# Kernel tuning notes

Hardware: AMD Instinct MI355X
Metric: run time of the kernel (lower is better)

## Reference

```python
import jax, jax.numpy as jnp
import numpy as np

DT = 0.1       # integration step (ms)
TAU_M = 10.0   # membrane time constant
TAU_S = 5.0    # synaptic time constant
E_REV = 1.0    # synaptic reversal potential
G_MAX = 1.0    # synaptic conductance scale
P, N, E, B, T = 8, 2048, 16, 4, 128


def setup_inputs() -> dict:
    key = jax.random.key(0)
    k_src, k_tgt, k_w, k_win = jax.random.split(key, 4)
    t_seq = jnp.arange(B * T, dtype=jnp.float32).reshape(B, T) * DT  # [B,T] times in ms
    src = jax.random.randint(k_src, (E,), 0, P, dtype=jnp.int32)
    tgt = jax.random.randint(k_tgt, (E,), 0, P, dtype=jnp.int32)
    W = jax.random.normal(k_w, (E, N, N), jnp.float32) * (1.0 / np.sqrt(N))
    W_in = jax.random.normal(k_win, (N, N), jnp.float32) * (1.0 / np.sqrt(N))
    v0 = jnp.zeros((P, B, N), jnp.float32)      # population states
    s0 = jnp.zeros((E, B, N), jnp.float32)      # recurrent synapse states
    s_in0 = jnp.zeros((B, N), jnp.float32)      # input synapse state
    return dict(t_seq=t_seq, W=W, W_in=W_in, v0=v0, s0=s0, s_in0=s_in0, src=src, tgt=tgt)


def _input_rate(t, n):
    # InputPopulation: firing rate is a pure function of time t, per-unit phase.
    phase = jnp.arange(n, dtype=jnp.float32) * (2.0 * jnp.pi / n)
    return 0.5 * (1.0 + jnp.sin(2.0 * jnp.pi * t[:, None] / 100.0 + phase[None, :]))  # [B,n]


def _simulate(t_seq, W, W_in, v0, s0, s_in0, src, tgt):
    n_pop = v0.shape[0]

    def step(carry, t):  # t: [B] current time
        v, s, s_in, err = carry
        rates = jax.nn.sigmoid(v)                      # [P,B,N] firing rates
        # --- synapse message passing: gather pre rates, dense projection ---
        pre = rates[src]                               # [E,B,N]
        drive = jnp.einsum('ebi,eij->ebj', pre, W)     # [E,B,N]
        s_new = s + DT * (-s / TAU_S + drive)          # exponential synapse state
        # --- input population synapse (pre rate is a function of t) ---
        rate_in = _input_rate(t, v.shape[-1])          # [B,N]
        s_in_new = s_in + DT * (-s_in / TAU_S + rate_in @ W_in)
        # --- conductance-based currents scattered into target populations ---
        post_v = v[tgt]                                # [E,B,N]
        I_e = G_MAX * s_new * (E_REV - post_v)
        g_e = G_MAX * s_new
        I_sum = jax.ops.segment_sum(I_e, tgt, num_segments=n_pop)  # [P,B,N]
        g_sum = jax.ops.segment_sum(g_e, tgt, num_segments=n_pop)
        I_in = G_MAX * s_in_new * (E_REV - v[0])
        I_sum = I_sum.at[0].add(I_in)
        g_sum = g_sum.at[0].add(G_MAX * s_in_new)
        # --- Euler integrator step + stability error accumulation ---
        dv = (-v - g_sum * v + I_sum) / TAU_M
        v_new = v + DT * dv
        err_new = err + jnp.mean(jnp.abs(dv)) * DT
        return (v_new, s_new, s_in_new, err_new), jax.nn.sigmoid(v_new)

    init = (v0, s0, s_in0, jnp.zeros((), jnp.float32))
    (v_f, s_f, s_in_f, err), rates_seq = jax.lax.scan(step, init, t_seq.T)  # rates_seq: [T,P,B,N]
    firing_rates = jnp.transpose(rates_seq, (2, 0, 1, 3))  # [B,T,P,N]
    return firing_rates, err


def reference(t_seq, W, W_in, v0, s0, s_in0, src, tgt):
    return _simulate(t_seq, W, W_in, v0, s0, s_in0, src, tgt)
```

## Files before the change

### kernel.cpp

```cpp
#include <hip/hip_runtime.h>
#include <math.h>

#define DT_     0.1f
#define TAU_M_  10.0f
#define TAU_S_  5.0f
#define NP_     8
#define NN_     2048
#define NE_     16
#define NB_     4
#define NT_     128
#define NEDGE_  17

typedef unsigned int u32;
typedef __attribute__((ext_vector_type(2))) _Float16 half2v;

__device__ __forceinline__ float sigmoidf_(float x) {
  return 1.0f / (1.0f + expf(-x));
}

__device__ __forceinline__ float dot2_(float acc, u32 p, u32 w) {
#if __has_builtin(__builtin_amdgcn_fdot2)
  return __builtin_amdgcn_fdot2(__builtin_bit_cast(half2v, p),
                                __builtin_bit_cast(half2v, w), acc, false);
#else
  half2v hp = __builtin_bit_cast(half2v, p);
  half2v hw = __builtin_bit_cast(half2v, w);
  return acc + (float)hp[0] * (float)hw[0] + (float)hp[1] * (float)hw[1];
#endif
}

__global__ __launch_bounds__(256) void k_transpose(
    const float* __restrict__ W, const float* __restrict__ W_in,
    u32* __restrict__ Wt32) {
  const int e  = blockIdx.x;
  const int jt = blockIdx.y;
  const int it = blockIdx.z;
  const float* Wsrc = (e == 16) ? W_in : (W + (size_t)e * NN_ * NN_);
  __shared__ float tile[64][65];
  const int i0 = it * 64, j0 = jt * 64;
  for (int k = threadIdx.x; k < 4096; k += 256) {
    int r = k >> 6, c = k & 63;
    tile[r][c] = Wsrc[(size_t)(i0 + r) * NN_ + j0 + c];
  }
  __syncthreads();
  for (int k = threadIdx.x; k < 2048; k += 256) {
    int jr = k >> 5, ip = k & 31;
    half2v h;
    h[0] = (_Float16)tile[2 * ip][jr];
    h[1] = (_Float16)tile[2 * ip + 1][jr];
    Wt32[((size_t)e * NN_ + (j0 + jr)) * 1024 + (i0 >> 1) + ip] =
        __builtin_bit_cast(u32, h);
  }
}

__global__ __launch_bounds__(256) void k_inrate(
    const float* __restrict__ t_seq, u32* __restrict__ inp) {
  const int t = blockIdx.x >> 2, b = blockIdx.x & 3;
  const float tt = t_seq[b * NT_ + t];
  const float base = 0.062831853071795864f * tt;
  for (int p2 = threadIdx.x; p2 < 1024; p2 += 256) {
    int i = 2 * p2;
    float ph0 = (float)i * (6.2831853071795864f / (float)NN_);
    float ph1 = (float)(i + 1) * (6.2831853071795864f / (float)NN_);
    half2v h;
    h[0] = (_Float16)(0.5f * (1.0f + sinf(base + ph0)));
    h[1] = (_Float16)(0.5f * (1.0f + sinf(base + ph1)));
    inp[(size_t)(t * NB_ + b) * 1024 + p2] = __builtin_bit_cast(u32, h);
  }
}

__global__ __launch_bounds__(256) void k_rates0(
    const float* __restrict__ v0, _Float16* __restrict__ rh0) {
  int idx = blockIdx.x * 256 + threadIdx.x;
  rh0[idx] = (_Float16)sigmoidf_(v0[idx]);
}

__global__ __launch_bounds__(256) void k_init(
    const float* __restrict__ v0, const float* __restrict__ s0,
    const float* __restrict__ s_in0,
    float* __restrict__ vg, float* __restrict__ sg,
    float* __restrict__ sig, float* __restrict__ errw) {
  int idx = blockIdx.x * 256 + threadIdx.x;
  if (idx < NE_ * NB_ * NN_) sg[idx] = s0[idx];
  if (idx < NP_ * NB_ * NN_) vg[idx] = v0[idx];
  if (idx < NB_ * NN_) sig[idx] = s_in0[idx];
  if (idx < NN_) errw[idx] = 0.0f;
}

__global__ __launch_bounds__(256) void k_step(
    const u32* __restrict__ Wt32, const u32* __restrict__ inp,
    const int* __restrict__ srcg, const int* __restrict__ tgtg,
    const u32* __restrict__ rcur, u32* __restrict__ rnext,
    float* __restrict__ sg_, float* __restrict__ sig_,
    float* __restrict__ vg_, float* __restrict__ errw,
    float* __restrict__ out, int t) {
  const int tid  = threadIdx.x;
  const int lane = tid & 63;
  const int wv   = tid >> 6;
  const int j    = blockIdx.x * 4 + wv;

  __shared__ u32 pairs_u[NB_ * 1024];

  float s_reg  = sg_[(size_t)lane * NN_ + j];
  float si_reg = (lane < 4) ? sig_[(size_t)lane * NN_ + j] : 0.0f;

  u32 streg[16];
  {
    const u32* rp = rcur + (size_t)srcg[0] * 4096 + tid * 16;
#pragma unroll
    for (int c = 0; c < 4; ++c) {
      uint4 q = *(const uint4*)(rp + c * 4);
      streg[c * 4 + 0] = q.x; streg[c * 4 + 1] = q.y;
      streg[c * 4 + 2] = q.z; streg[c * 4 + 3] = q.w;
    }
  }

  for (int E = 0; E < NEDGE_; ++E) {
    bool do_stage = (E == 0) || (E == 16) || (srcg[E] != srcg[E - 1]);
    if (do_stage) {
      __syncthreads();
#pragma unroll
      for (int c = 0; c < 4; ++c) {
        uint4 q = {streg[c * 4 + 0], streg[c * 4 + 1],
                   streg[c * 4 + 2], streg[c * 4 + 3]};
        *(uint4*)(&pairs_u[tid * 16 + c * 4]) = q;
      }
      __syncthreads();
    }
    if (E < 16) {
      bool next_stage = (E + 1 == 16) || (srcg[E + 1] != srcg[E]);
      if (next_stage) {
        const u32* np = (E + 1 == 16)
            ? (inp + (size_t)t * NB_ * 1024 + tid * 16)
            : (rcur + (size_t)srcg[E + 1] * 4096 + tid * 16);
#pragma unroll
        for (int c = 0; c < 4; ++c) {
          uint4 q = *(const uint4*)(np + c * 4);
          streg[c * 4 + 0] = q.x; streg[c * 4 + 1] = q.y;
          streg[c * 4 + 2] = q.z; streg[c * 4 + 3] = q.w;
        }
      }
    }

    const u32* wp = Wt32 + ((size_t)E * NN_ + j) * 1024;
    float acc0 = 0.0f, acc1 = 0.0f, acc2 = 0.0f, acc3 = 0.0f;
#pragma unroll
    for (int c = 0; c < 4; ++c) {
      const int base = c * 256 + lane * 4;
      uint4 w = *(const uint4*)(wp + base);
      uint4 p0 = *(const uint4*)(&pairs_u[base]);
      uint4 p1 = *(const uint4*)(&pairs_u[1024 + base]);
      uint4 p2 = *(const uint4*)(&pairs_u[2048 + base]);
      uint4 p3 = *(const uint4*)(&pairs_u[3072 + base]);
      acc0 = dot2_(dot2_(dot2_(dot2_(acc0, p0.x, w.x), p0.y, w.y), p0.z, w.z), p0.w, w.w);
      acc1 = dot2_(dot2_(dot2_(dot2_(acc1, p1.x, w.x), p1.y, w.y), p1.z, w.z), p1.w, w.w);
      acc2 = dot2_(dot2_(dot2_(dot2_(acc2, p2.x, w.x), p2.y, w.y), p2.z, w.z), p2.w, w.w);
      acc3 = dot2_(dot2_(dot2_(dot2_(acc3, p3.x, w.x), p3.y, w.y), p3.z, w.z), p3.w, w.w);
    }

    float t0 = acc0 + __shfl_xor(acc0, 1, 64);
    float t1 = acc1 + __shfl_xor(acc1, 1, 64);
    float t2 = acc2 + __shfl_xor(acc2, 1, 64);
    float t3 = acc3 + __shfl_xor(acc3, 1, 64);
    float u0 = (lane & 1) ? t1 : t0;
    float u2 = (lane & 1) ? t3 : t2;
    u0 = u0 + __shfl_xor(u0, 2, 64);
    u2 = u2 + __shfl_xor(u2, 2, 64);
    float r = (lane & 2) ? u2 : u0;
    r += __shfl_xor(r, 4, 64);
    r += __shfl_xor(r, 8, 64);
    r += __shfl_xor(r, 16, 64);
    r += __shfl_xor(r, 32, 64);

    if (E < NE_) {
      if ((lane >> 2) == E) s_reg += DT_ * (r - s_reg * (1.0f / TAU_S_));
    } else {
      if (lane < 4) si_reg += DT_ * (r - si_reg * (1.0f / TAU_S_));
    }
  }

  sg_[(size_t)lane * NN_ + j] = s_reg;
  if (lane < 4) sig_[(size_t)lane * NN_ + j] = si_reg;

  {
    const int p = lane >> 2, b = lane & 3;
    float S = 0.0f;
#pragma unroll
    for (int e = 0; e < NE_; ++e) {
      float se = __shfl(s_reg, e * 4 + b, 64);
      if (tgtg[e] == p) S += se;
    }
    float sival = __shfl(si_reg, b, 64);
    if (p == 0) S += sival;

    float vv = (lane < 32) ? vg_[(size_t)lane * NN_ + j] : 0.0f;
    float I  = S * (1.0f - vv);
    float dv = (-vv - S * vv + I) * (1.0f / TAU_M_);
    float vn = vv + DT_ * dv;
    float rr = sigmoidf_(vn);
    if (lane < 32) {
      vg_[(size_t)lane * NN_ + j] = vn;
      ((_Float16*)rnext)[(size_t)lane * NN_ + j] = (_Float16)rr;
      out[(((size_t)b * NT_ + t) * NP_ + p) * NN_ + j] = rr;
    }
    float ea = (lane < 32) ? fabsf(dv) : 0.0f;
#pragma unroll
    for (int off = 1; off < 64; off <<= 1) ea += __shfl_xor(ea, off, 64);
    if (lane == 0) errw[j] += ea;
  }
}

__global__ __launch_bounds__(256) void k_err(
    const float* __restrict__ errw, float* __restrict__ out_err) {
  __shared__ float red[256];
  float s = 0.0f;
  for (int k = threadIdx.x; k < NN_; k += 256) s += errw[k];
  red[threadIdx.x] = s;
  __syncthreads();
  for (int w = 128; w > 0; w >>= 1) {
    if (threadIdx.x < w) red[threadIdx.x] += red[threadIdx.x + w];
    __syncthreads();
  }
  if (threadIdx.x == 0)
    *out_err = red[0] * (DT_ / (float)(NP_ * NB_ * NN_));
}

extern "C" void kernel_launch(void* const* d_in, const int* in_sizes, int n_in,
                              void* d_out, int out_size, void* d_ws, size_t ws_size,
                              hipStream_t stream) {
  const float* t_seq = (const float*)d_in[0];
  const float* W     = (const float*)d_in[1];
  const float* W_in  = (const float*)d_in[2];
  const float* v0    = (const float*)d_in[3];
  const float* s0    = (const float*)d_in[4];
  const float* s_in0 = (const float*)d_in[5];
  const int*   srcp  = (const int*)d_in[6];
  const int*   tgtp  = (const int*)d_in[7];
  float* outp = (float*)d_out;

  u32* Wt32 = (u32*)d_ws;
  u32* inp  = Wt32 + (size_t)NEDGE_ * NN_ * 1024;
  u32* rb0  = inp + (size_t)NT_ * NB_ * 1024;
  u32* rb1  = rb0 + (size_t)NP_ * NB_ * 1024;
  float* sg   = (float*)(rb1 + (size_t)NP_ * NB_ * 1024);
  float* vg   = sg + (size_t)NE_ * NB_ * NN_;
  float* sig  = vg + (size_t)NP_ * NB_ * NN_;
  float* errw = sig + (size_t)NB_ * NN_;

  hipLaunchKernelGGL(k_transpose, dim3(NEDGE_, 32, 32), dim3(256), 0, stream,
                     W, W_in, Wt32);
  hipLaunchKernelGGL(k_inrate, dim3(NT_ * NB_), dim3(256), 0, stream,
                     t_seq, inp);
  hipLaunchKernelGGL(k_rates0, dim3(256), dim3(256), 0, stream,
                     v0, (_Float16*)rb0);
  hipLaunchKernelGGL(k_init, dim3(512), dim3(256), 0, stream,
                     v0, s0, s_in0, vg, sg, sig, errw);

  u32* rb[2] = {rb0, rb1};
  for (int t = 0; t < NT_; ++t) {
    hipLaunchKernelGGL(k_step, dim3(512), dim3(256), 0, stream,
                       Wt32, inp, srcp, tgtp,
                       rb[t & 1], rb[(t + 1) & 1],
                       sg, sig, vg, errw, outp, t);
  }

  hipLaunchKernelGGL(k_err, dim3(1), dim3(256), 0, stream,
                     errw, outp + (size_t)NB_ * NT_ * NP_ * NN_);
}
```

Before: 3.677 ms.

## Hold pre-rates in registers per wave and software-pipeline weight loads

Shared-memory staging of the pre-synaptic rates and its block barriers are removed. Each wave now loads the whole 4x1024 packed rate vector it needs straight into registers, with redundant global/L2 reads across the block's four waves. Weight rows for the next edge are prefetched into registers while the current edge's dot products run, and launch bounds request two blocks per CU. This raises register pressure (about 64 rate registers plus double-buffered weights), which could cause spills or lower occupancy.

```diff
diff --git a/kernel.cpp b/kernel.cpp
--- a/kernel.cpp
+++ b/kernel.cpp
@@ -87,7 +87,7 @@
   if (idx < NN_) errw[idx] = 0.0f;
 }
 
-__global__ __launch_bounds__(256) void k_step(
+__global__ __launch_bounds__(256, 2) void k_step(
     const u32* __restrict__ Wt32, const u32* __restrict__ inp,
     const int* __restrict__ srcg, const int* __restrict__ tgtg,
     const u32* __restrict__ rcur, u32* __restrict__ rnext,
@@ -98,64 +98,59 @@
   const int lane = tid & 63;
   const int wv   = tid >> 6;
   const int j    = blockIdx.x * 4 + wv;
-
-  __shared__ u32 pairs_u[NB_ * 1024];
+  const int l4   = lane * 4;
 
   float s_reg  = sg_[(size_t)lane * NN_ + j];
   float si_reg = (lane < 4) ? sig_[(size_t)lane * NN_ + j] : 0.0f;
 
-  u32 streg[16];
+  uint4 r0[4], r1[4], r2[4], r3[4];
   {
-    const u32* rp = rcur + (size_t)srcg[0] * 4096 + tid * 16;
+    const u32* rp = rcur + (size_t)srcg[0] * 4096 + l4;
 #pragma unroll
     for (int c = 0; c < 4; ++c) {
-      uint4 q = *(const uint4*)(rp + c * 4);
-      streg[c * 4 + 0] = q.x; streg[c * 4 + 1] = q.y;
-      streg[c * 4 + 2] = q.z; streg[c * 4 + 3] = q.w;
-    }
-  }
-
+      r0[c] = *(const uint4*)(rp + c * 256);
+      r1[c] = *(const uint4*)(rp + 1024 + c * 256);
+      r2[c] = *(const uint4*)(rp + 2048 + c * 256);
+      r3[c] = *(const uint4*)(rp + 3072 + c * 256);
+    }
+  }
+  uint4 wq[4];
+#pragma unroll
+  for (int c = 0; c < 4; ++c)
+    wq[c] = *(const uint4*)(Wt32 + (size_t)j * 1024 + c * 256 + l4);
+
+#pragma unroll
   for (int E = 0; E < NEDGE_; ++E) {
-    bool do_stage = (E == 0) || (E == 16) || (srcg[E] != srcg[E - 1]);
-    if (do_stage) {
-      __syncthreads();
-#pragma unroll
-      for (int c = 0; c < 4; ++c) {
-        uint4 q = {streg[c * 4 + 0], streg[c * 4 + 1],
-                   streg[c * 4 + 2], streg[c * 4 + 3]};
-        *(uint4*)(&pairs_u[tid * 16 + c * 4]) = q;
-      }
-      __syncthreads();
-    }
-    if (E < 16) {
-      bool next_stage = (E + 1 == 16) || (srcg[E + 1] != srcg[E]);
-      if (next_stage) {
-        const u32* np = (E + 1 == 16)
-            ? (inp + (size_t)t * NB_ * 1024 + tid * 16)
-            : (rcur + (size_t)srcg[E + 1] * 4096 + tid * 16);
+    uint4 wn[4];
+    if (E + 1 < NEDGE_) {
+      const u32* wp = Wt32 + ((size_t)(E + 1) * NN_ + j) * 1024 + l4;
+#pragma unroll
+      for (int c = 0; c < 4; ++c) wn[c] = *(const uint4*)(wp + c * 256);
+    }
+
+    float acc0 = 0.0f, acc1 = 0.0f, acc2 = 0.0f, acc3 = 0.0f;
+#pragma unroll
+    for (int c = 0; c < 4; ++c) {
+      uint4 w = wq[c];
+      acc0 = dot2_(dot2_(dot2_(dot2_(acc0, r0[c].x, w.x), r0[c].y, w.y), r0[c].z, w.z), r0[c].w, w.w);
+      acc1 = dot2_(dot2_(dot2_(dot2_(acc1, r1[c].x, w.x), r1[c].y, w.y), r1[c].z, w.z), r1[c].w, w.w);
+      acc2 = dot2_(dot2_(dot2_(dot2_(acc2, r2[c].x, w.x), r2[c].y, w.y), r2[c].z, w.z), r2[c].w, w.w);
+      acc3 = dot2_(dot2_(dot2_(dot2_(acc3, r3[c].x, w.x), r3[c].y, w.y), r3[c].z, w.z), r3[c].w, w.w);
+    }
+
+    if (E + 1 < NEDGE_) {
+      bool next_in = (E + 1 == 16);
+      if (next_in || srcg[E + 1] != srcg[E]) {
+        const u32* np = next_in ? (inp + (size_t)t * NB_ * 1024 + l4)
+                                : (rcur + (size_t)srcg[E + 1] * 4096 + l4);
 #pragma unroll
         for (int c = 0; c < 4; ++c) {
-          uint4 q = *(const uint4*)(np + c * 4);
-          streg[c * 4 + 0] = q.x; streg[c * 4 + 1] = q.y;
-          streg[c * 4 + 2] = q.z; streg[c * 4 + 3] = q.w;
+          r0[c] = *(const uint4*)(np + c * 256);
+          r1[c] = *(const uint4*)(np + 1024 + c * 256);
+          r2[c] = *(const uint4*)(np + 2048 + c * 256);
+          r3[c] = *(const uint4*)(np + 3072 + c * 256);
         }
       }
-    }
-
-    const u32* wp = Wt32 + ((size_t)E * NN_ + j) * 1024;
-    float acc0 = 0.0f, acc1 = 0.0f, acc2 = 0.0f, acc3 = 0.0f;
-#pragma unroll
-    for (int c = 0; c < 4; ++c) {
-      const int base = c * 256 + lane * 4;
-      uint4 w = *(const uint4*)(wp + base);
-      uint4 p0 = *(const uint4*)(&pairs_u[base]);
-      uint4 p1 = *(const uint4*)(&pairs_u[1024 + base]);
-      uint4 p2 = *(const uint4*)(&pairs_u[2048 + base]);
-      uint4 p3 = *(const uint4*)(&pairs_u[3072 + base]);
-      acc0 = dot2_(dot2_(dot2_(dot2_(acc0, p0.x, w.x), p0.y, w.y), p0.z, w.z), p0.w, w.w);
-      acc1 = dot2_(dot2_(dot2_(dot2_(acc1, p1.x, w.x), p1.y, w.y), p1.z, w.z), p1.w, w.w);
-      acc2 = dot2_(dot2_(dot2_(dot2_(acc2, p2.x, w.x), p2.y, w.y), p2.z, w.z), p2.w, w.w);
-      acc3 = dot2_(dot2_(dot2_(dot2_(acc3, p3.x, w.x), p3.y, w.y), p3.z, w.z), p3.w, w.w);
     }
 
     float t0 = acc0 + __shfl_xor(acc0, 1, 64);
@@ -177,6 +172,9 @@
     } else {
       if (lane < 4) si_reg += DT_ * (r - si_reg * (1.0f / TAU_S_));
     }
+
+#pragma unroll
+    for (int c = 0; c < 4; ++c) wq[c] = wn[c];
   }
 
   sg_[(size_t)lane * NN_ + j] = s_reg;
```

Result: slower. 3.824 ms (+4.0%).
